# Kernel optimization log

Measured on AMD Instinct MI355X. Metric: run time of the kernel, lower is better.

The kernel has to match this reference:

```python
import jax, jax.numpy as jnp
import numpy as np

B, C, H, W = 1, 96, 128, 128
P = 4            # patch_size
E = 192          # embed_dim
DI = 384         # d_inner = expand * embed_dim
NS = 16          # d_state
R = 12           # dt_rank = ceil(E/16)
K = 4            # scan directions
NBLK = 8         # SS2D_MBs_num
GW = C // 2      # SCPA group width


def layernorm(x, g, b, eps=1e-5):
    mu = x.mean(-1, keepdims=True)
    v = x.var(-1, keepdims=True)
    return (x - mu) * jax.lax.rsqrt(v + eps) * g + b


def batchnorm(x, g, b, m, v, eps=1e-5):
    # eval-mode BatchNorm2d over channel axis 1 of (B,C,H,W)
    return (x - m[:, None, None]) * jax.lax.rsqrt(v + eps)[:, None, None] * g[:, None, None] + b[:, None, None]


def conv2d(x, w):
    return jax.lax.conv_general_dilated(x, w, (1, 1), 'SAME', dimension_numbers=('NCHW', 'OIHW', 'NCHW'))


def dwconv2d(x, w, b):
    out = jax.lax.conv_general_dilated(x, w[:, None], (1, 1), 'SAME',
                                       dimension_numbers=('NCHW', 'OIHW', 'NCHW'),
                                       feature_group_count=w.shape[0])
    return out + b[None, :, None, None]


def lrelu(x):
    return jnp.where(x >= 0, x, 0.2 * x)


def channel_attention(x, w1, w2):
    # CBAM-style: shared MLP on avg+max pooled channel descriptors, sigmoid gate
    avg = x.mean((2, 3))
    mx = x.max((2, 3))
    mlp = lambda v: jax.nn.relu(v @ w1.T) @ w2.T
    attn = jax.nn.sigmoid(mlp(avg) + mlp(mx))
    return x * attn[:, :, None, None]


def selective_scan(xs, dts, A, Bs, Cs, Dskip):
    # xs,dts: (B,K,DI,L); A: (K,DI,NS); Bs,Cs: (B,K,NS,L); Dskip: (K,DI)
    xs_t = jnp.moveaxis(xs, -1, 0)
    dts_t = jnp.moveaxis(dts, -1, 0)
    Bs_t = jnp.moveaxis(Bs, -1, 0)
    Cs_t = jnp.moveaxis(Cs, -1, 0)
    h0 = jnp.zeros(xs.shape[:3] + (NS,), xs.dtype)  # (B,K,DI,NS)

    def step(h, t):
        xt, dt, Bt, Ct = t
        h = jnp.exp(dt[..., None] * A) * h + (dt * xt)[..., None] * Bt[:, :, None, :]
        return h, jnp.sum(h * Ct[:, :, None, :], axis=-1)

    _, ys = jax.lax.scan(step, h0, (xs_t, dts_t, Bs_t, Cs_t))
    return jnp.moveaxis(ys, 0, -1) + xs * Dskip[None, :, :, None]


def ss2d_block(x, p):
    # VMamba-style VSS block: x + SS2D(LN(x)); x: (B,Hp,Wp,E)
    (ln_g, ln_b, inproj_w, conv_w, conv_b, xproj_w, dtproj_w, dtproj_b,
     Alog, Dskip, on_g, on_b, outproj_w, merge_w) = p
    Bsz, Hp, Wp, _ = x.shape
    L = Hp * Wp
    h = layernorm(x, ln_g, ln_b)
    xz = jnp.einsum('bhwd,ed->bhwe', h, inproj_w)   # (B,Hp,Wp,2*DI)
    xc, z = jnp.split(xz, 2, axis=-1)
    xc = jax.nn.silu(dwconv2d(jnp.transpose(xc, (0, 3, 1, 2)), conv_w, conv_b))  # (B,DI,Hp,Wp)
    # 4-direction cross-scan: row-major, col-major and their reverses
    xf = xc.reshape(Bsz, DI, L)
    xwh = jnp.transpose(xc, (0, 1, 3, 2)).reshape(Bsz, DI, L)
    xs = jnp.stack([xf, xwh, jnp.flip(xf, -1), jnp.flip(xwh, -1)], axis=1)  # (B,K,DI,L)
    x_dbl = jnp.einsum('bkdl,kcd->bkcl', xs, xproj_w)  # (B,K,R+2*NS,L)
    dts, Bm, Cm = jnp.split(x_dbl, [R, R + NS], axis=2)
    dts = jax.nn.softplus(jnp.einsum('bkrl,kdr->bkdl', dts, dtproj_w) + dtproj_b[None, :, :, None])
    A = -jnp.exp(Alog)
    oy = selective_scan(xs, dts, A, Bm, Cm, Dskip)  # (B,K,DI,L)
    y0 = oy[:, 0]
    y1 = jnp.transpose(oy[:, 1].reshape(Bsz, DI, Wp, Hp), (0, 1, 3, 2)).reshape(Bsz, DI, L)
    y2 = jnp.flip(oy[:, 2], -1)
    y3 = jnp.transpose(jnp.flip(oy[:, 3], -1).reshape(Bsz, DI, Wp, Hp), (0, 1, 3, 2)).reshape(Bsz, DI, L)
    y = merge_w[0] * y0 + merge_w[1] * y1 + merge_w[2] * y2 + merge_w[3] * y3  # learnable merge
    y = jnp.transpose(y, (0, 2, 1)).reshape(Bsz, Hp, Wp, DI)
    y = layernorm(y, on_g, on_b) * jax.nn.silu(z)
    return x + jnp.einsum('bhwd,ed->bhwe', y, outproj_w)


def scpa(x, c1a, c1b, k1, k2w, k2b, k3, k4, c3):
    # PAN SCPA: two branches (3x3 conv / pixel-attention conv), 1x1 fuse, residual
    a = lrelu(jnp.einsum('bchw,oc->bohw', x, c1a))
    b = lrelu(jnp.einsum('bchw,oc->bohw', x, c1b))
    a = conv2d(a, k1)
    g = jax.nn.sigmoid(jnp.einsum('bchw,oc->bohw', b, k2w) + k2b[None, :, None, None])
    b = conv2d(conv2d(b, k3) * g, k4)
    out = jnp.einsum('bchw,oc->bohw', jnp.concatenate([lrelu(a), lrelu(b)], 1), c3)
    return out + x


def _forward(x, bn1_g, bn1_b, bn1_m, bn1_v, ca_w1, ca_w2, pe_w, pe_b, pu_w, pu_b,
             blk_ln_g, blk_ln_b, blk_inproj_w, blk_conv_w, blk_conv_b, blk_xproj_w,
             blk_dtproj_w, blk_dtproj_b, blk_Alog, blk_D, blk_on_g, blk_on_b,
             blk_outproj_w, blk_merge_w, bn2_g, bn2_b, bn2_m, bn2_v,
             scpa_c1a_w, scpa_c1b_w, scpa_k1_w, pa_k2_w, pa_k2_b, pa_k3_w, pa_k4_w, scpa_c3_w):
    residual = x
    h = batchnorm(x, bn1_g, bn1_b, bn1_m, bn1_v)
    x1 = channel_attention(h, ca_w1, ca_w2)
    Hp, Wp = H // P, W // P
    # patch embed: (B,C,H,W) -> (B,Hp,Wp,C*P*P) -> linear -> (B,Hp,Wp,E)
    xp = h.reshape(B, C, Hp, P, Wp, P).transpose(0, 2, 4, 1, 3, 5).reshape(B, Hp, Wp, C * P * P)
    x2 = xp @ pe_w.T + pe_b
    blk_params = (blk_ln_g, blk_ln_b, blk_inproj_w, blk_conv_w, blk_conv_b, blk_xproj_w,
                  blk_dtproj_w, blk_dtproj_b, blk_Alog, blk_D, blk_on_g, blk_on_b,
                  blk_outproj_w, blk_merge_w)
    x2, _ = jax.lax.scan(lambda c, p: (ss2d_block(c, p), None), x2, blk_params)
    # patch unembed
    xu = x2 @ pu_w.T + pu_b
    xu = xu.reshape(B, Hp, Wp, C, P, P).transpose(0, 3, 1, 4, 2, 5).reshape(B, C, H, W)
    xsum = residual + x1 + xu
    h2 = batchnorm(xsum, bn2_g, bn2_b, bn2_m, bn2_v)
    out = scpa(h2, scpa_c1a_w, scpa_c1b_w, scpa_k1_w, pa_k2_w, pa_k2_b, pa_k3_w, pa_k4_w, scpa_c3_w)
    return out + xsum


def setup_inputs():
    key = jax.random.key(0)
    kct = [0]
    def nk():
        kct[0] += 1
        return jax.random.fold_in(key, kct[0])
    def nrm(shape, s=0.02):
        return (jax.random.normal(nk(), shape) * s).astype(jnp.float32)
    f32 = jnp.float32
    inp = dict(
        x=jax.random.normal(nk(), (B, C, H, W), dtype=f32),
        bn1_g=jnp.ones((C,), f32), bn1_b=jnp.zeros((C,), f32),
        bn1_m=nrm((C,), 0.05), bn1_v=jnp.ones((C,), f32),
        ca_w1=nrm((C // 16, C), 0.1), ca_w2=nrm((C, C // 16), 0.1),
        pe_w=nrm((E, C * P * P)), pe_b=jnp.zeros((E,), f32),
        pu_w=nrm((C * P * P, E)), pu_b=jnp.zeros((C * P * P,), f32),
        blk_ln_g=jnp.ones((NBLK, E), f32), blk_ln_b=jnp.zeros((NBLK, E), f32),
        blk_inproj_w=nrm((NBLK, 2 * DI, E)),
        blk_conv_w=nrm((NBLK, DI, 3, 3), 0.1),
        blk_conv_b=jnp.zeros((NBLK, DI), f32),
        blk_xproj_w=nrm((NBLK, K, R + 2 * NS, DI)),
        blk_dtproj_w=nrm((NBLK, K, DI, R), 0.1),
        blk_dtproj_b=jnp.full((NBLK, K, DI), -4.6, f32),  # softplus ~= 0.01
        blk_Alog=jnp.broadcast_to(jnp.log(jnp.arange(1, NS + 1, dtype=f32)), (NBLK, K, DI, NS)) + 0.0,
        blk_D=jnp.ones((NBLK, K, DI), f32),
        blk_on_g=jnp.ones((NBLK, DI), f32), blk_on_b=jnp.zeros((NBLK, DI), f32),
        blk_outproj_w=nrm((NBLK, E, DI)),
        blk_merge_w=jnp.ones((NBLK, K), f32),
        bn2_g=jnp.ones((C,), f32), bn2_b=jnp.zeros((C,), f32),
        bn2_m=nrm((C,), 0.05), bn2_v=jnp.ones((C,), f32),
        scpa_c1a_w=nrm((GW, C), 0.05), scpa_c1b_w=nrm((GW, C), 0.05),
        scpa_k1_w=nrm((GW, GW, 3, 3), 0.05),
        pa_k2_w=nrm((GW, GW), 0.05), pa_k2_b=jnp.zeros((GW,), f32),
        pa_k3_w=nrm((GW, GW, 3, 3), 0.05), pa_k4_w=nrm((GW, GW, 3, 3), 0.05),
        scpa_c3_w=nrm((C, 2 * GW), 0.05),
    )
    return inp


def reference(x, bn1_g, bn1_b, bn1_m, bn1_v, ca_w1, ca_w2, pe_w, pe_b, pu_w, pu_b,
              blk_ln_g, blk_ln_b, blk_inproj_w, blk_conv_w, blk_conv_b, blk_xproj_w,
              blk_dtproj_w, blk_dtproj_b, blk_Alog, blk_D, blk_on_g, blk_on_b,
              blk_outproj_w, blk_merge_w, bn2_g, bn2_b, bn2_m, bn2_v,
              scpa_c1a_w, scpa_c1b_w, scpa_k1_w, pa_k2_w, pa_k2_b, pa_k3_w, pa_k4_w, scpa_c3_w):
    return _forward(x, bn1_g, bn1_b, bn1_m, bn1_v, ca_w1, ca_w2, pe_w, pe_b, pu_w, pu_b,
                    blk_ln_g, blk_ln_b, blk_inproj_w, blk_conv_w, blk_conv_b, blk_xproj_w,
                    blk_dtproj_w, blk_dtproj_b, blk_Alog, blk_D, blk_on_g, blk_on_b,
                    blk_outproj_w, blk_merge_w, bn2_g, bn2_b, bn2_m, bn2_v,
                    scpa_c1a_w, scpa_c1b_w, scpa_k1_w, pa_k2_w, pa_k2_b, pa_k3_w, pa_k4_w, scpa_c3_w)
```

## Files before the change

kernel.cpp:

```cpp
#include <hip/hip_runtime.h>
#include <math.h>

#define HW 16384
constexpr int C_ = 96;
constexpr int E_ = 192, DI_ = 384, NS_ = 16, R_ = 12, K_ = 4, NBLK_ = 8, GW_ = 48;
constexpr int L_ = 1024, CXP_ = 44;
constexpr int TC_ = 64;
constexpr int NCH_ = L_ / TC_;

__device__ __forceinline__ float lrelu_(float x){ return x >= 0.f ? x : 0.2f*x; }
__device__ __forceinline__ float sigmoid_(float x){ return 1.f/(1.f+expf(-x)); }
__device__ __forceinline__ float silu_(float x){ return x/(1.f+expf(-x)); }
__device__ __forceinline__ float softplus_(float x){ return fmaxf(x,0.f)+log1pf(expf(-fabsf(x))); }

__global__ void k_transpose(const float* __restrict__ in, float* __restrict__ out,
                            int rows, int cols, int in_stride){
  __shared__ float t[32][33];
  const float* ib = in + (size_t)blockIdx.z*rows*in_stride;
  float* ob = out + (size_t)blockIdx.z*rows*cols;
  int r0 = blockIdx.y*32, c0 = blockIdx.x*32;
  int tx = threadIdx.x, ty = threadIdx.y;
  for (int i=0;i<32;i+=8){
    int r = r0+ty+i, c = c0+tx;
    if (r<rows && c<cols) t[ty+i][tx] = ib[(size_t)r*in_stride+c];
  }
  __syncthreads();
  for (int i=0;i<32;i+=8){
    int c = c0+ty+i, r = r0+tx;
    if (r<rows && c<cols) ob[(size_t)c*rows+r] = t[tx][ty+i];
  }
}

__global__ void k_bn1(const float* __restrict__ x, const float* g, const float* b,
                      const float* m, const float* v,
                      float* __restrict__ h, float* __restrict__ stats){
  int c = blockIdx.x, tid = threadIdx.x;
  float sc = g[c]*rsqrtf(v[c]+1e-5f), sh = b[c]-m[c]*sc;
  const float* xc = x + (size_t)c*HW;
  float* hc = h + (size_t)c*HW;
  float s = 0.f, mx = -1e30f;
  for (int i=tid;i<HW;i+=256){
    float val = fmaf(xc[i], sc, sh);
    hc[i] = val; s += val; mx = fmaxf(mx, val);
  }
  for (int o=32;o;o>>=1){ s += __shfl_xor(s,o); mx = fmaxf(mx, __shfl_xor(mx,o)); }
  __shared__ float ss[4], sm[4];
  int wid = tid>>6, lane = tid&63;
  if (!lane){ ss[wid]=s; sm[wid]=mx; }
  __syncthreads();
  if (!tid){
    stats[c] = (ss[0]+ss[1]+ss[2]+ss[3])*(1.f/HW);
    stats[96+c] = fmaxf(fmaxf(sm[0],sm[1]),fmaxf(sm[2],sm[3]));
  }
}

__global__ void k_attn(const float* __restrict__ stats, const float* __restrict__ w1,
                       const float* __restrict__ w2, float* __restrict__ attn){
  __shared__ float hid[12];
  int tid = threadIdx.x;
  if (tid < 12){
    int j = tid%6, which = tid/6;
    const float* vv = stats + which*96;
    float a = 0.f;
    for (int c=0;c<96;c++) a += vv[c]*w1[j*96+c];
    hid[tid] = fmaxf(a, 0.f);
  }
  __syncthreads();
  if (tid < 96){
    float a = 0.f;
    for (int j=0;j<6;j++) a += (hid[j]+hid[6+j])*w2[tid*6+j];
    attn[tid] = sigmoid_(a);
  }
}

__global__ void k_patchify(const float* __restrict__ h, float* __restrict__ xp){
  int idx = blockIdx.x*256 + threadIdx.x;
  int l = idx/1536, kk = idx%1536;
  int c = kk>>4, i = (kk>>2)&3, j = kk&3;
  int hp = l>>5, wp = l&31;
  xp[idx] = h[((size_t)c<<14) + (size_t)(hp*4+i)*128 + (wp*4+j)];
}

__global__ __launch_bounds__(256) void k_gemm32(const float* __restrict__ act,
                      const float* __restrict__ wt, const float* __restrict__ bias,
                      const float* __restrict__ res, float* __restrict__ out,
                      int K, int N){
  __shared__ float As[32][34];
  __shared__ float Bs[32][32];
  int tid = threadIdx.x;
  int m0 = blockIdx.x*32, n0 = blockIdx.y*32;
  int tx = tid&15, ty = tid>>4;
  int arow = tid>>3, akq = tid&7;
  int brow = tid>>3, bn4 = tid&7;
  float4 aR = *(const float4*)&act[(size_t)(m0+arow)*K + akq*4];
  float4 bR = *(const float4*)&wt [(size_t)brow*N + n0 + bn4*4];
  float acc[2][2] = {{0}};
  for (int k0=0; k0<K; k0+=32){
    __syncthreads();
    As[akq*4+0][arow]=aR.x; As[akq*4+1][arow]=aR.y;
    As[akq*4+2][arow]=aR.z; As[akq*4+3][arow]=aR.w;
    *(float4*)&Bs[brow][bn4*4] = bR;
    __syncthreads();
    if (k0+32 < K){
      aR = *(const float4*)&act[(size_t)(m0+arow)*K + k0+32 + akq*4];
      bR = *(const float4*)&wt [(size_t)(k0+32+brow)*N + n0 + bn4*4];
    }
    #pragma unroll
    for (int kk=0; kk<32; kk++){
      float2 av = *(const float2*)&As[kk][ty*2];
      float2 bv = *(const float2*)&Bs[kk][tx*2];
      acc[0][0] = fmaf(av.x, bv.x, acc[0][0]);
      acc[0][1] = fmaf(av.x, bv.y, acc[0][1]);
      acc[1][0] = fmaf(av.y, bv.x, acc[1][0]);
      acc[1][1] = fmaf(av.y, bv.y, acc[1][1]);
    }
  }
  float2 bq = bias ? *(const float2*)&bias[n0+tx*2] : make_float2(0.f,0.f);
  #pragma unroll
  for (int i=0;i<2;i++){
    size_t o = (size_t)(m0+ty*2+i)*N + n0 + tx*2;
    float2 r = res ? *(const float2*)&res[o] : make_float2(0.f,0.f);
    float2 ov;
    ov.x = acc[i][0]+bq.x+r.x; ov.y = acc[i][1]+bq.y+r.y;
    *(float2*)&out[o] = ov;
  }
}

__global__ void k_lnstats(const float* __restrict__ x, float* __restrict__ mu,
                          float* __restrict__ rs){
  int l = blockIdx.x*4 + (threadIdx.x>>6);
  int lane = threadIdx.x&63;
  const float* xr = x + (size_t)l*E_;
  float v0 = xr[lane], v1 = xr[lane+64], v2 = xr[lane+128];
  float s = v0+v1+v2, sq = v0*v0+v1*v1+v2*v2;
  for (int o=32;o;o>>=1){ s += __shfl_xor(s,o); sq += __shfl_xor(sq,o); }
  if (!lane){
    float m = s*(1.f/192.f);
    mu[l] = m;
    rs[l] = rsqrtf(sq*(1.f/192.f) - m*m + 1e-5f);
  }
}

__global__ __launch_bounds__(256) void k_gemm32ln(const float* __restrict__ act,
                      const float* __restrict__ wt, const float* __restrict__ lg,
                      const float* __restrict__ lb, const float* __restrict__ mu,
                      const float* __restrict__ rs, float* __restrict__ out,
                      int K, int N){
  __shared__ float As[32][34];
  __shared__ float Bs[32][32];
  int tid = threadIdx.x;
  int m0 = blockIdx.x*32, n0 = blockIdx.y*32;
  int tx = tid&15, ty = tid>>4;
  int arow = tid>>3, akq = tid&7;
  int brow = tid>>3, bn4 = tid&7;
  float m = mu[m0+arow], r = rs[m0+arow];
  float4 aR = *(const float4*)&act[(size_t)(m0+arow)*K + akq*4];
  float4 gR = *(const float4*)&lg[akq*4];
  float4 hR = *(const float4*)&lb[akq*4];
  float4 bR = *(const float4*)&wt[(size_t)brow*N + n0 + bn4*4];
  float acc[2][2] = {{0}};
  for (int k0=0; k0<K; k0+=32){
    __syncthreads();
    As[akq*4+0][arow] = (aR.x-m)*r*gR.x + hR.x;
    As[akq*4+1][arow] = (aR.y-m)*r*gR.y + hR.y;
    As[akq*4+2][arow] = (aR.z-m)*r*gR.z + hR.z;
    As[akq*4+3][arow] = (aR.w-m)*r*gR.w + hR.w;
    *(float4*)&Bs[brow][bn4*4] = bR;
    __syncthreads();
    if (k0+32 < K){
      aR = *(const float4*)&act[(size_t)(m0+arow)*K + k0+32 + akq*4];
      gR = *(const float4*)&lg[k0+32+akq*4];
      hR = *(const float4*)&lb[k0+32+akq*4];
      bR = *(const float4*)&wt[(size_t)(k0+32+brow)*N + n0 + bn4*4];
    }
    #pragma unroll
    for (int kk=0; kk<32; kk++){
      float2 av = *(const float2*)&As[kk][ty*2];
      float2 bv = *(const float2*)&Bs[kk][tx*2];
      acc[0][0] = fmaf(av.x, bv.x, acc[0][0]);
      acc[0][1] = fmaf(av.x, bv.y, acc[0][1]);
      acc[1][0] = fmaf(av.y, bv.x, acc[1][0]);
      acc[1][1] = fmaf(av.y, bv.y, acc[1][1]);
    }
  }
  #pragma unroll
  for (int i=0;i<2;i++){
    size_t o = (size_t)(m0+ty*2+i)*N + n0 + tx*2;
    float2 ov; ov.x = acc[i][0]; ov.y = acc[i][1];
    *(float2*)&out[o] = ov;
  }
}

__global__ __launch_bounds__(256) void k_dwxst(const float* __restrict__ xz,
                        const float* __restrict__ w, const float* __restrict__ bias,
                        float* __restrict__ xcs, float* __restrict__ xst){
  __shared__ float ld[96][33];
  __shared__ float t[32][33];
  int h0 = blockIdx.x;
  int d0 = blockIdx.y*32;
  int tx = threadIdx.x, ty = threadIdx.y;
  #pragma unroll
  for (int i=0;i<12;i++){
    int ll = i*8 + ty;
    int h = h0 - 1 + (ll>>5);
    int wv = ll & 31;
    float v = 0.f;
    if ((unsigned)h < 32u) v = xz[(size_t)(h*32+wv)*768 + d0 + tx];
    ld[ll][tx] = v;
  }
  __syncthreads();
  #pragma unroll
  for (int i=0;i<4;i++){
    int dl = ty + 8*i;
    int d = d0 + dl;
    float acc = bias[d];
    const float* wp = w + d*9;
    #pragma unroll
    for (int di=0;di<3;di++){
      #pragma unroll
      for (int dj=0;dj<3;dj++){
        int wq = tx + dj - 1;
        if ((unsigned)wq < 32u)
          acc = fmaf(ld[di*32 + wq][dl], wp[di*3+dj], acc);
      }
    }
    float val = silu_(acc);
    xcs[(size_t)d*L_ + h0*32 + tx] = val;
    t[dl][tx] = val;
  }
  __syncthreads();
  int d = d0 + tx;
  #pragma unroll
  for (int i=0;i<4;i++){
    int wq = ty + 8*i;
    int l = h0*32 + wq;
    float val = t[tx][wq];
    int t1 = wq*32 + h0;
    xst[(size_t)l*DI_ + d] = val;
    xst[(size_t)(L_ + t1)*DI_ + d] = val;
    xst[(size_t)(2*L_ + (1023-l))*DI_ + d] = val;
    xst[(size_t)(3*L_ + (1023-t1))*DI_ + d] = val;
  }
}

__global__ __launch_bounds__(256) void k_xdblP(const float* __restrict__ xcs,
                       const float* __restrict__ xw, float* __restrict__ xdblP){
  int kz = blockIdx.z;
  int k = kz & 3, sp = kz >> 2;
  int s = blockIdx.x*256 + threadIdx.x;
  int Ts = ((s&31)<<5) | (s>>5);
  int lw;
  if (k==0) lw = s;
  else if (k==1) lw = Ts;
  else if (k==2) lw = 1023-s;
  else lw = 1023-Ts;
  int c0 = blockIdx.y*4;
  const float* wp = xw + ((size_t)k*CXP_ + c0)*DI_ + sp*128;
  const float* src = xcs + s + (size_t)sp*128*L_;
  float a0=0,a1=0,a2=0,a3=0;
  for (int d=0; d<128; d++){
    float v = src[(size_t)d*L_];
    a0 = fmaf(v, wp[d],        a0);
    a1 = fmaf(v, wp[DI_+d],    a1);
    a2 = fmaf(v, wp[2*DI_+d],  a2);
    a3 = fmaf(v, wp[3*DI_+d],  a3);
  }
  size_t base = (((size_t)sp*4 + k)*CXP_ + c0)*L_ + lw;
  xdblP[base]       = a0;
  xdblP[base+L_]    = a1;
  xdblP[base+2*L_]  = a2;
  xdblP[base+3*L_]  = a3;
}

__global__ void k_dtbc(const float* __restrict__ xdblP, const float* __restrict__ dtw,
                       const float* __restrict__ dtb, float* __restrict__ dts_t,
                       float* __restrict__ bc){
  int k = blockIdx.y, l = blockIdx.x, d = threadIdx.x;
  const float* p0 = xdblP + ((size_t)(0+k)*CXP_)*L_ + l;
  const float* p1 = xdblP + ((size_t)(4+k)*CXP_)*L_ + l;
  const float* p2 = xdblP + ((size_t)(8+k)*CXP_)*L_ + l;
  float acc = dtb[(size_t)k*DI_ + d];
  const float* w = dtw + ((size_t)k*DI_ + d)*R_;
  #pragma unroll
  for (int r=0;r<R_;r++){
    size_t o = (size_t)r*L_;
    acc = fmaf(p0[o]+p1[o]+p2[o], w[r], acc);
  }
  dts_t[((size_t)k*L_ + l)*DI_ + d] = softplus_(acc);
  if (d < 32){
    size_t o = (size_t)(R_+d)*L_;
    bc[((size_t)k*L_ + l)*32 + d] = p0[o]+p1[o]+p2[o];
  }
}

__global__ __launch_bounds__(256) void k_scanA(const float* __restrict__ xst,
                      const float* __restrict__ dts_t, const float* __restrict__ bc,
                      const float* __restrict__ Alog,
                      float* __restrict__ Ech, float* __restrict__ Hch){
  int k = blockIdx.z;
  int d = blockIdx.y*16 + (threadIdx.x>>4);
  int n = threadIdx.x&15;
  int ch = blockIdx.x;
  float A = -expf(Alog[((size_t)k*DI_ + d)*NS_ + n]);
  float aL2 = A * 1.4426950408889634f;
  int t0 = ch*TC_;
  const float* dtp = dts_t + ((size_t)k*L_ + t0)*DI_ + d;
  const float* xp_ = xst   + ((size_t)k*L_ + t0)*DI_ + d;
  const float* bcp = bc    + ((size_t)k*L_ + t0)*32;
  float h = 0.f, Ep = 1.f;
  #pragma unroll 4
  for (int t=0;t<TC_;t++){
    float dt = dtp[(size_t)t*DI_];
    float xv = xp_[(size_t)t*DI_];
    float Bn = bcp[t*32+n];
    float e = exp2f(aL2*dt);
    h = fmaf(e, h, dt*xv*Bn);
    Ep *= e;
  }
  size_t idx = (((size_t)k*NCH_ + ch)*DI_ + d)*NS_ + n;
  Ech[idx] = Ep; Hch[idx] = h;
}

__global__ void k_scanB(const float* __restrict__ Ech, const float* __restrict__ Hch,
                        float* __restrict__ carry){
  int idx = blockIdx.x*256 + threadIdx.x;
  int k = idx / (DI_*NS_);
  int dn = idx % (DI_*NS_);
  float h = 0.f;
  #pragma unroll
  for (int c=0;c<NCH_;c++){
    size_t o = ((size_t)(k*NCH_+c)*DI_*NS_) + dn;
    carry[o] = h;
    h = fmaf(Ech[o], h, Hch[o]);
  }
}

__global__ __launch_bounds__(256) void k_scanC(const float* __restrict__ xst,
                      const float* __restrict__ dts_t, const float* __restrict__ bc,
                      const float* __restrict__ Alog, const float* __restrict__ carry,
                      float* __restrict__ yst){
  int k = blockIdx.z;
  int d = blockIdx.y*16 + (threadIdx.x>>4);
  int n = threadIdx.x&15;
  int ch = blockIdx.x;
  float A = -expf(Alog[((size_t)k*DI_ + d)*NS_ + n]);
  float aL2 = A * 1.4426950408889634f;
  int t0 = ch*TC_;
  const float* dtp = dts_t + ((size_t)k*L_ + t0)*DI_ + d;
  const float* xp_ = xst   + ((size_t)k*L_ + t0)*DI_ + d;
  const float* bcp = bc    + ((size_t)k*L_ + t0)*32;
  float* yp = yst + ((size_t)k*L_ + t0)*DI_ + d;
  float h = carry[(((size_t)k*NCH_ + ch)*DI_ + d)*NS_ + n];
  #pragma unroll 4
  for (int t=0;t<TC_;t++){
    float dt = dtp[(size_t)t*DI_];
    float xv = xp_[(size_t)t*DI_];
    float Bn = bcp[t*32+n], Cn = bcp[t*32+16+n];
    float e = exp2f(aL2*dt);
    h = fmaf(e, h, dt*xv*Bn);
    float p = h*Cn;
    p += __shfl_xor(p,1); p += __shfl_xor(p,2);
    p += __shfl_xor(p,4); p += __shfl_xor(p,8);
    if (n==0) yp[(size_t)t*DI_] = p;
  }
}

__global__ void k_merge(const float* __restrict__ yst, const float* __restrict__ xst,
                        const float* __restrict__ Dsk, const float* __restrict__ mw,
                        const float* __restrict__ ong, const float* __restrict__ onb,
                        const float* __restrict__ xz, float* __restrict__ out){
  int l = blockIdx.x, d = threadIdx.x;
  int T = ((l&31)<<5) | (l>>5);
  int tt[4] = { l, T, 1023-l, 1023-T };
  float v = 0.f;
  #pragma unroll
  for (int k=0;k<4;k++){
    size_t idx = (size_t)(k*L_ + tt[k])*DI_ + d;
    v += mw[k]*(yst[idx] + xst[idx]*Dsk[k*DI_+d]);
  }
  float s = v, sq = v*v;
  for (int o=32;o;o>>=1){ s += __shfl_xor(s,o); sq += __shfl_xor(sq,o); }
  __shared__ float rs_[6], rq_[6];
  int lane = d&63, wid = d>>6;
  if (!lane){ rs_[wid]=s; rq_[wid]=sq; }
  __syncthreads();
  float ts=0.f, tq=0.f;
  #pragma unroll
  for (int i=0;i<6;i++){ ts += rs_[i]; tq += rq_[i]; }
  float mu = ts*(1.f/DI_);
  float rstd = rsqrtf(tq*(1.f/DI_) - mu*mu + 1e-5f);
  float y = (v-mu)*rstd*ong[d] + onb[d];
  float z = xz[(size_t)l*768 + DI_ + d];
  out[(size_t)l*DI_ + d] = y * silu_(z);
}

__global__ void k_sum(const float* __restrict__ x, const float* __restrict__ h,
                      const float* __restrict__ attn, const float* __restrict__ xu,
                      const float* g2, const float* b2, const float* m2, const float* v2,
                      float* __restrict__ xsum, float* __restrict__ h2){
  int idx = blockIdx.x*256 + threadIdx.x;
  int c = idx>>14, p = idx&16383;
  int hh = p>>7, ww = p&127;
  int l = (hh>>2)*32 + (ww>>2);
  int o = (c<<4) + ((hh&3)<<2) + (ww&3);
  float s = x[idx] + h[idx]*attn[c] + xu[(size_t)l*1536 + o];
  xsum[idx] = s;
  h2[idx] = (s - m2[c])*rsqrtf(v2[c]+1e-5f)*g2[c] + b2[c];
}

__global__ __launch_bounds__(256) void k_1x1ab(const float* __restrict__ h2,
                        const float* __restrict__ wa, const float* __restrict__ wb,
                        float* __restrict__ a, float* __restrict__ b){
  __shared__ float lw[96*12];
  int ocg = blockIdx.x;
  for (int i=threadIdx.x; i<96*12; i+=256){
    int o = i%12, c = i/12;
    lw[i] = (o<6) ? wa[(ocg*6 + o)*96 + c] : wb[(ocg*6 + (o-6))*96 + c];
  }
  __syncthreads();
  int p = blockIdx.y*256 + threadIdx.x;
  float acc[12];
  #pragma unroll
  for (int o=0;o<12;o++) acc[o]=0.f;
  for (int c=0;c<96;c++){
    float v = h2[(size_t)c*HW + p];
    const float* w = lw + c*12;
    #pragma unroll
    for (int o=0;o<12;o++) acc[o] = fmaf(v, w[o], acc[o]);
  }
  #pragma unroll
  for (int o=0;o<6;o++){
    a[(size_t)(ocg*6+o)*HW + p] = lrelu_(acc[o]);
    b[(size_t)(ocg*6+o)*HW + p] = lrelu_(acc[6+o]);
  }
}

__global__ __launch_bounds__(256) void k_1x1g(const float* __restrict__ b,
                       const float* __restrict__ w, const float* __restrict__ bias,
                       float* __restrict__ g){
  __shared__ float lw[48*6];
  int ocg = blockIdx.x;
  for (int i=threadIdx.x; i<48*6; i+=256){
    int o = i%6, c = i/6;
    lw[i] = w[(ocg*6 + o)*48 + c];
  }
  __syncthreads();
  int p = blockIdx.y*256 + threadIdx.x;
  float acc[6];
  #pragma unroll
  for (int o=0;o<6;o++) acc[o] = bias[ocg*6+o];
  for (int c=0;c<48;c++){
    float v = b[(size_t)c*HW + p];
    const float* wp = lw + c*6;
    #pragma unroll
    for (int o=0;o<6;o++) acc[o] = fmaf(v, wp[o], acc[o]);
  }
  #pragma unroll
  for (int o=0;o<6;o++) g[(size_t)(ocg*6+o)*HW + p] = sigmoid_(acc[o]);
}

__global__ __launch_bounds__(256) void k_conv3(const float* __restrict__ in,
                        const float* __restrict__ w, const float* __restrict__ aux,
                        float* __restrict__ out, int mode){
  __shared__ float lw[48*9*6];
  int ocg = blockIdx.x;
  for (int i=threadIdx.x; i<48*9*6; i+=256){
    int o = i%6, j = (i/6)%9, ic = i/54;
    lw[i] = w[((size_t)(ocg*6+o)*48 + ic)*9 + j];
  }
  __syncthreads();
  int p = blockIdx.y*256 + threadIdx.x;
  int hh = p>>7, ww = p&127;
  float acc[6];
  #pragma unroll
  for (int o=0;o<6;o++) acc[o]=0.f;
  for (int ic=0; ic<48; ic++){
    const float* ip = in + (size_t)ic*HW;
    float xv[9];
    #pragma unroll
    for (int di=0;di<3;di++){
      int y = hh+di-1;
      bool yok = (unsigned)y < 128u;
      #pragma unroll
      for (int dj=0;dj<3;dj++){
        int xx = ww+dj-1;
        bool ok = yok && ((unsigned)xx < 128u);
        xv[di*3+dj] = ok ? ip[y*128+xx] : 0.f;
      }
    }
    const float* lwp = lw + ic*54;
    #pragma unroll
    for (int j=0;j<9;j++){
      float xj = xv[j];
      const float* wj = lwp + j*6;
      #pragma unroll
      for (int o=0;o<6;o++) acc[o] = fmaf(xj, wj[o], acc[o]);
    }
  }
  #pragma unroll
  for (int o=0;o<6;o++){
    size_t oi = (size_t)(ocg*6+o)*HW + p;
    out[oi] = (mode==0) ? lrelu_(acc[o]) : acc[o]*aux[oi];
  }
}

__global__ __launch_bounds__(256) void k_c3(const float* __restrict__ ab,
                     const float* __restrict__ w, const float* __restrict__ h2,
                     const float* __restrict__ xsum, float* __restrict__ out){
  __shared__ float lw[96*12];
  int ocg = blockIdx.x;
  for (int i=threadIdx.x; i<96*12; i+=256){
    int o = i%12, j = i/12;
    lw[i] = w[(ocg*12 + o)*96 + j];
  }
  __syncthreads();
  int p = blockIdx.y*256 + threadIdx.x;
  float acc[12];
  #pragma unroll
  for (int o=0;o<12;o++) acc[o]=0.f;
  for (int j=0;j<96;j++){
    float v = ab[(size_t)j*HW + p];
    const float* wp = lw + j*12;
    #pragma unroll
    for (int o=0;o<12;o++) acc[o] = fmaf(v, wp[o], acc[o]);
  }
  #pragma unroll
  for (int o=0;o<12;o++){
    size_t oi = (size_t)(ocg*12+o)*HW + p;
    out[oi] = acc[o] + h2[oi] + xsum[oi];
  }
}

extern "C" void kernel_launch(void* const* d_in, const int* in_sizes, int n_in,
                              void* d_out, int out_size, void* d_ws, size_t ws_size,
                              hipStream_t stream){
  (void)in_sizes; (void)n_in; (void)out_size; (void)ws_size;
  const float* x    = (const float*)d_in[0];
  const float* bn1g = (const float*)d_in[1];
  const float* bn1b = (const float*)d_in[2];
  const float* bn1m = (const float*)d_in[3];
  const float* bn1v = (const float*)d_in[4];
  const float* caw1 = (const float*)d_in[5];
  const float* caw2 = (const float*)d_in[6];
  const float* peW  = (const float*)d_in[7];
  const float* peb  = (const float*)d_in[8];
  const float* puW  = (const float*)d_in[9];
  const float* pub  = (const float*)d_in[10];
  const float* lng  = (const float*)d_in[11];
  const float* lnb  = (const float*)d_in[12];
  const float* inW  = (const float*)d_in[13];
  const float* convw= (const float*)d_in[14];
  const float* convb= (const float*)d_in[15];
  const float* xprojw=(const float*)d_in[16];
  const float* dtw  = (const float*)d_in[17];
  const float* dtb  = (const float*)d_in[18];
  const float* Alog = (const float*)d_in[19];
  const float* Dsk  = (const float*)d_in[20];
  const float* ong  = (const float*)d_in[21];
  const float* onb  = (const float*)d_in[22];
  const float* outW = (const float*)d_in[23];
  const float* mw   = (const float*)d_in[24];
  const float* bn2g = (const float*)d_in[25];
  const float* bn2b = (const float*)d_in[26];
  const float* bn2m = (const float*)d_in[27];
  const float* bn2v = (const float*)d_in[28];
  const float* c1a  = (const float*)d_in[29];
  const float* c1b  = (const float*)d_in[30];
  const float* k1w  = (const float*)d_in[31];
  const float* k2w  = (const float*)d_in[32];
  const float* k2b  = (const float*)d_in[33];
  const float* k3w  = (const float*)d_in[34];
  const float* k4w  = (const float*)d_in[35];
  const float* c3w  = (const float*)d_in[36];
  float* out = (float*)d_out;

  float* ws = (float*)d_ws;
  size_t off = 0;
  auto alloc = [&](size_t n){ float* p = ws + off; off += n; return p; };
  float* peWT  = alloc((size_t)1536*192);
  float* puWT  = alloc((size_t)192*1536);
  float* inWT  = alloc((size_t)8*192*768);
  float* outWT = alloc((size_t)8*384*192);
  float* bufH  = alloc((size_t)96*HW);
  float* stats = alloc(256);
  float* attn  = alloc(128);
  float* bufP  = alloc((size_t)1024*1536);
  float* x2a   = alloc((size_t)1024*192);
  float* x2b   = alloc((size_t)1024*192);
  float* bufXZ = alloc((size_t)1024*768);
  float* bufXCS= alloc((size_t)384*1024);
  float* bufXST= alloc((size_t)4*1024*384);
  float* xdblP = alloc((size_t)12*44*1024);
  float* dts   = alloc((size_t)4*1024*384);
  float* bc    = alloc((size_t)4*1024*32);
  float* yst   = alloc((size_t)4*1024*384);
  float* bufY  = alloc((size_t)1024*384);
  float* xsum  = alloc((size_t)96*HW);
  float* h2    = alloc((size_t)96*HW);
  float* Ech   = alloc((size_t)K_*NCH_*DI_*NS_);
  float* Hch   = alloc((size_t)K_*NCH_*DI_*NS_);
  float* carry = alloc((size_t)K_*NCH_*DI_*NS_);
  float* muB   = alloc(1024);
  float* rsB   = alloc(1024);

  dim3 tb(32,8);
  k_transpose<<<dim3(48,6,1), tb, 0, stream>>>(peW, peWT, 192, 1536, 1536);
  k_transpose<<<dim3(6,48,1), tb, 0, stream>>>(puW, puWT, 1536, 192, 192);
  k_transpose<<<dim3(6,24,8), tb, 0, stream>>>(inW, inWT, 768, 192, 192);
  k_transpose<<<dim3(12,6,8), tb, 0, stream>>>(outW, outWT, 192, 384, 384);

  k_bn1<<<96,256,0,stream>>>(x, bn1g, bn1b, bn1m, bn1v, bufH, stats);
  k_attn<<<1,128,0,stream>>>(stats, caw1, caw2, attn);
  k_patchify<<<(1024*1536)/256,256,0,stream>>>(bufH, bufP);
  k_gemm32<<<dim3(32,6),256,0,stream>>>(bufP, peWT, peb, nullptr, x2a, 1536, 192);

  float* cur = x2a; float* nxt = x2b;
  for (int b=0;b<8;b++){
    k_lnstats<<<256,256,0,stream>>>(cur, muB, rsB);
    k_gemm32ln<<<dim3(32,24),256,0,stream>>>(cur, inWT+(size_t)b*192*768,
                        lng+(size_t)b*192, lnb+(size_t)b*192, muB, rsB, bufXZ, 192, 768);
    k_dwxst<<<dim3(32,12),tb,0,stream>>>(bufXZ, convw+(size_t)b*384*9,
                        convb+(size_t)b*384, bufXCS, bufXST);
    k_xdblP<<<dim3(4,11,12),256,0,stream>>>(bufXCS, xprojw+(size_t)b*4*44*384, xdblP);
    k_dtbc<<<dim3(1024,4),384,0,stream>>>(xdblP, dtw+(size_t)b*4*384*12, dtb+(size_t)b*4*384, dts, bc);
    const float* Ab = Alog + (size_t)b*4*384*16;
    k_scanA<<<dim3(NCH_,DI_/16,4),256,0,stream>>>(bufXST, dts, bc, Ab, Ech, Hch);
    k_scanB<<<(K_*DI_*NS_)/256,256,0,stream>>>(Ech, Hch, carry);
    k_scanC<<<dim3(NCH_,DI_/16,4),256,0,stream>>>(bufXST, dts, bc, Ab, carry, yst);
    k_merge<<<1024,384,0,stream>>>(yst, bufXST, Dsk+(size_t)b*4*384, mw+(size_t)b*4,
                                   ong+(size_t)b*384, onb+(size_t)b*384, bufXZ, bufY);
    k_gemm32<<<dim3(32,6),256,0,stream>>>(bufY, outWT+(size_t)b*384*192, nullptr, cur, nxt, 384, 192);
    float* t = cur; cur = nxt; nxt = t;
  }

  k_gemm32<<<dim3(32,48),256,0,stream>>>(cur, puWT, pub, nullptr, bufP, 192, 1536);
  k_sum<<<(96*HW)/256,256,0,stream>>>(x, bufH, attn, bufP, bn2g, bn2b, bn2m, bn2v, xsum, h2);

  float* bufA = dts;
  float* bufB = dts + (size_t)48*HW;
  float* bufG = yst;
  float* bufT = yst + (size_t)48*HW;
  float* ab   = bufXST;
  k_1x1ab<<<dim3(8,64),256,0,stream>>>(h2, c1a, c1b, bufA, bufB);
  k_1x1g<<<dim3(8,64),256,0,stream>>>(bufB, k2w, k2b, bufG);
  k_conv3<<<dim3(8,64),256,0,stream>>>(bufA, k1w, nullptr, ab, 0);
  k_conv3<<<dim3(8,64),256,0,stream>>>(bufB, k3w, bufG, bufT, 1);
  k_conv3<<<dim3(8,64),256,0,stream>>>(bufT, k4w, nullptr, ab+(size_t)48*HW, 0);
  k_c3<<<dim3(8,64),256,0,stream>>>(ab, c3w, h2, xsum, out);
}
```

Before: 1.161 ms.

## Fuse patchify, unpatchify and LN stats into GEMMs; dedupe scan inputs; tile conv3 in LDS

Several independent changes land together. Patchify is folded into the patch-embed GEMM's A loads, and the unpatchify scatter is moved into the patch-unembed GEMM's epilogue. The per-block LayerNorm statistics kernel is removed: row sum and sum-of-squares are accumulated with atomics in the residual GEMM epilogue, and the merge kernel zeroes the accumulators for the next use. The four direction-permuted copies of the scan input become two, with reversed directions read via a negative stride. The 3x3 conv now stages input rows in shared memory. Together these cut launches and memory traffic, at the cost of atomics, an E[x^2]-m^2 variance form, and extra per-channel syncs in the conv.

```diff
diff --git a/kernel.cpp b/kernel.cpp
--- a/kernel.cpp
+++ b/kernel.cpp
@@ -33,8 +33,11 @@
 
 __global__ void k_bn1(const float* __restrict__ x, const float* g, const float* b,
                       const float* m, const float* v,
-                      float* __restrict__ h, float* __restrict__ stats){
+                      float* __restrict__ h, float* __restrict__ stats,
+                      float* __restrict__ su, float* __restrict__ sq){
   int c = blockIdx.x, tid = threadIdx.x;
+  int gid = c*256 + tid;
+  if (gid < 1024){ su[gid] = 0.f; sq[gid] = 0.f; }
   float sc = g[c]*rsqrtf(v[c]+1e-5f), sh = b[c]-m[c]*sc;
   const float* xc = x + (size_t)c*HW;
   float* hc = h + (size_t)c*HW;
@@ -73,17 +76,69 @@
   }
 }
 
-__global__ void k_patchify(const float* __restrict__ h, float* __restrict__ xp){
-  int idx = blockIdx.x*256 + threadIdx.x;
-  int l = idx/1536, kk = idx%1536;
-  int c = kk>>4, i = (kk>>2)&3, j = kk&3;
-  int hp = l>>5, wp = l&31;
-  xp[idx] = h[((size_t)c<<14) + (size_t)(hp*4+i)*128 + (wp*4+j)];
-}
-
-__global__ __launch_bounds__(256) void k_gemm32(const float* __restrict__ act,
+__global__ __launch_bounds__(256) void k_gemmPE(const float* __restrict__ hsrc,
                       const float* __restrict__ wt, const float* __restrict__ bias,
-                      const float* __restrict__ res, float* __restrict__ out,
+                      float* __restrict__ out, float* __restrict__ su, float* __restrict__ sq){
+  const int K = 1536, N = 192;
+  __shared__ float As[32][34];
+  __shared__ float Bs[32][32];
+  int tid = threadIdx.x;
+  int m0 = blockIdx.x*32, n0 = blockIdx.y*32;
+  int tx = tid&15, ty = tid>>4;
+  int arow = tid>>3, akq = tid&7;
+  int brow = tid>>3, bn4 = tid&7;
+  int m = m0+arow;
+  int base2 = (m>>5)*512 + (m&31)*4;
+  auto aload = [&](int kk)->float4 {
+    int c = kk>>4, i2 = (kk>>2)&3;
+    return *(const float4*)&hsrc[((size_t)c<<14) + (size_t)(i2*128 + base2)];
+  };
+  float4 aR = aload(akq*4);
+  float4 bR = *(const float4*)&wt[(size_t)brow*N + n0 + bn4*4];
+  float acc[2][2] = {{0}};
+  for (int k0=0; k0<K; k0+=32){
+    __syncthreads();
+    As[akq*4+0][arow]=aR.x; As[akq*4+1][arow]=aR.y;
+    As[akq*4+2][arow]=aR.z; As[akq*4+3][arow]=aR.w;
+    *(float4*)&Bs[brow][bn4*4] = bR;
+    __syncthreads();
+    if (k0+32 < K){
+      aR = aload(k0+32+akq*4);
+      bR = *(const float4*)&wt[(size_t)(k0+32+brow)*N + n0 + bn4*4];
+    }
+    #pragma unroll
+    for (int kk=0; kk<32; kk++){
+      float2 av = *(const float2*)&As[kk][ty*2];
+      float2 bv = *(const float2*)&Bs[kk][tx*2];
+      acc[0][0] = fmaf(av.x, bv.x, acc[0][0]);
+      acc[0][1] = fmaf(av.x, bv.y, acc[0][1]);
+      acc[1][0] = fmaf(av.y, bv.x, acc[1][0]);
+      acc[1][1] = fmaf(av.y, bv.y, acc[1][1]);
+    }
+  }
+  float2 bq = *(const float2*)&bias[n0+tx*2];
+  float sl[2], ql[2];
+  #pragma unroll
+  for (int i=0;i<2;i++){
+    size_t o = (size_t)(m0+ty*2+i)*N + n0 + tx*2;
+    float2 ov; ov.x = acc[i][0]+bq.x; ov.y = acc[i][1]+bq.y;
+    *(float2*)&out[o] = ov;
+    sl[i] = ov.x+ov.y; ql[i] = ov.x*ov.x+ov.y*ov.y;
+  }
+  #pragma unroll
+  for (int o=8;o;o>>=1){
+    sl[0]+=__shfl_xor(sl[0],o); ql[0]+=__shfl_xor(ql[0],o);
+    sl[1]+=__shfl_xor(sl[1],o); ql[1]+=__shfl_xor(ql[1],o);
+  }
+  if (tx==0){
+    atomicAdd(&su[m0+ty*2],   sl[0]); atomicAdd(&sq[m0+ty*2],   ql[0]);
+    atomicAdd(&su[m0+ty*2+1], sl[1]); atomicAdd(&sq[m0+ty*2+1], ql[1]);
+  }
+}
+
+__global__ __launch_bounds__(256) void k_gemm32s(const float* __restrict__ act,
+                      const float* __restrict__ wt, const float* __restrict__ res,
+                      float* __restrict__ out, float* __restrict__ su, float* __restrict__ sq,
                       int K, int N){
   __shared__ float As[32][34];
   __shared__ float Bs[32][32];
@@ -115,36 +170,76 @@
       acc[1][1] = fmaf(av.y, bv.y, acc[1][1]);
     }
   }
-  float2 bq = bias ? *(const float2*)&bias[n0+tx*2] : make_float2(0.f,0.f);
+  float sl[2], ql[2];
   #pragma unroll
   for (int i=0;i<2;i++){
     size_t o = (size_t)(m0+ty*2+i)*N + n0 + tx*2;
-    float2 r = res ? *(const float2*)&res[o] : make_float2(0.f,0.f);
-    float2 ov;
-    ov.x = acc[i][0]+bq.x+r.x; ov.y = acc[i][1]+bq.y+r.y;
+    float2 r = *(const float2*)&res[o];
+    float2 ov; ov.x = acc[i][0]+r.x; ov.y = acc[i][1]+r.y;
     *(float2*)&out[o] = ov;
-  }
-}
-
-__global__ void k_lnstats(const float* __restrict__ x, float* __restrict__ mu,
-                          float* __restrict__ rs){
-  int l = blockIdx.x*4 + (threadIdx.x>>6);
-  int lane = threadIdx.x&63;
-  const float* xr = x + (size_t)l*E_;
-  float v0 = xr[lane], v1 = xr[lane+64], v2 = xr[lane+128];
-  float s = v0+v1+v2, sq = v0*v0+v1*v1+v2*v2;
-  for (int o=32;o;o>>=1){ s += __shfl_xor(s,o); sq += __shfl_xor(sq,o); }
-  if (!lane){
-    float m = s*(1.f/192.f);
-    mu[l] = m;
-    rs[l] = rsqrtf(sq*(1.f/192.f) - m*m + 1e-5f);
+    sl[i] = ov.x+ov.y; ql[i] = ov.x*ov.x+ov.y*ov.y;
+  }
+  #pragma unroll
+  for (int o=8;o;o>>=1){
+    sl[0]+=__shfl_xor(sl[0],o); ql[0]+=__shfl_xor(ql[0],o);
+    sl[1]+=__shfl_xor(sl[1],o); ql[1]+=__shfl_xor(ql[1],o);
+  }
+  if (tx==0){
+    atomicAdd(&su[m0+ty*2],   sl[0]); atomicAdd(&sq[m0+ty*2],   ql[0]);
+    atomicAdd(&su[m0+ty*2+1], sl[1]); atomicAdd(&sq[m0+ty*2+1], ql[1]);
+  }
+}
+
+__global__ __launch_bounds__(256) void k_gemmPU(const float* __restrict__ act,
+                      const float* __restrict__ wt, const float* __restrict__ bias,
+                      float* __restrict__ out){
+  const int K = 192, N = 1536;
+  __shared__ float As[32][34];
+  __shared__ float Bs[32][32];
+  int tid = threadIdx.x;
+  int m0 = blockIdx.x*32, n0 = blockIdx.y*32;
+  int tx = tid&15, ty = tid>>4;
+  int arow = tid>>3, akq = tid&7;
+  int brow = tid>>3, bn4 = tid&7;
+  float4 aR = *(const float4*)&act[(size_t)(m0+arow)*K + akq*4];
+  float4 bR = *(const float4*)&wt [(size_t)brow*N + n0 + bn4*4];
+  float acc[2][2] = {{0}};
+  for (int k0=0; k0<K; k0+=32){
+    __syncthreads();
+    As[akq*4+0][arow]=aR.x; As[akq*4+1][arow]=aR.y;
+    As[akq*4+2][arow]=aR.z; As[akq*4+3][arow]=aR.w;
+    *(float4*)&Bs[brow][bn4*4] = bR;
+    __syncthreads();
+    if (k0+32 < K){
+      aR = *(const float4*)&act[(size_t)(m0+arow)*K + k0+32 + akq*4];
+      bR = *(const float4*)&wt [(size_t)(k0+32+brow)*N + n0 + bn4*4];
+    }
+    #pragma unroll
+    for (int kk=0; kk<32; kk++){
+      float2 av = *(const float2*)&As[kk][ty*2];
+      float2 bv = *(const float2*)&Bs[kk][tx*2];
+      acc[0][0] = fmaf(av.x, bv.x, acc[0][0]);
+      acc[0][1] = fmaf(av.x, bv.y, acc[0][1]);
+      acc[1][0] = fmaf(av.y, bv.x, acc[1][0]);
+      acc[1][1] = fmaf(av.y, bv.y, acc[1][1]);
+    }
+  }
+  int n = n0 + tx*2;
+  float2 bq = *(const float2*)&bias[n];
+  int c = n>>4, i2 = (n>>2)&3, j = n&3;
+  #pragma unroll
+  for (int i=0;i<2;i++){
+    int m = m0+ty*2+i;
+    size_t o = ((size_t)c<<14) + (size_t)((m>>5)*4+i2)*128 + (m&31)*4 + j;
+    float2 ov; ov.x = acc[i][0]+bq.x; ov.y = acc[i][1]+bq.y;
+    *(float2*)&out[o] = ov;
   }
 }
 
 __global__ __launch_bounds__(256) void k_gemm32ln(const float* __restrict__ act,
                       const float* __restrict__ wt, const float* __restrict__ lg,
-                      const float* __restrict__ lb, const float* __restrict__ mu,
-                      const float* __restrict__ rs, float* __restrict__ out,
+                      const float* __restrict__ lb, const float* __restrict__ su,
+                      const float* __restrict__ sq, float* __restrict__ out,
                       int K, int N){
   __shared__ float As[32][34];
   __shared__ float Bs[32][32];
@@ -153,7 +248,8 @@
   int tx = tid&15, ty = tid>>4;
   int arow = tid>>3, akq = tid&7;
   int brow = tid>>3, bn4 = tid&7;
-  float m = mu[m0+arow], r = rs[m0+arow];
+  float m = su[m0+arow]*(1.f/192.f);
+  float r = rsqrtf(sq[m0+arow]*(1.f/192.f) - m*m + 1e-5f);
   float4 aR = *(const float4*)&act[(size_t)(m0+arow)*K + akq*4];
   float4 gR = *(const float4*)&lg[akq*4];
   float4 hR = *(const float4*)&lb[akq*4];
@@ -193,7 +289,8 @@
 
 __global__ __launch_bounds__(256) void k_dwxst(const float* __restrict__ xz,
                         const float* __restrict__ w, const float* __restrict__ bias,
-                        float* __restrict__ xcs, float* __restrict__ xst){
+                        float* __restrict__ xcs, float* __restrict__ xst0,
+                        float* __restrict__ xst1){
   __shared__ float ld[96][33];
   __shared__ float t[32][33];
   int h0 = blockIdx.x;
@@ -236,10 +333,8 @@
     int l = h0*32 + wq;
     float val = t[tx][wq];
     int t1 = wq*32 + h0;
-    xst[(size_t)l*DI_ + d] = val;
-    xst[(size_t)(L_ + t1)*DI_ + d] = val;
-    xst[(size_t)(2*L_ + (1023-l))*DI_ + d] = val;
-    xst[(size_t)(3*L_ + (1023-t1))*DI_ + d] = val;
+    xst0[(size_t)l*DI_ + d] = val;
+    xst1[(size_t)t1*DI_ + d] = val;
   }
 }
 
@@ -293,7 +388,8 @@
   }
 }
 
-__global__ __launch_bounds__(256) void k_scanA(const float* __restrict__ xst,
+__global__ __launch_bounds__(256) void k_scanA(const float* __restrict__ xst0,
+                      const float* __restrict__ xst1,
                       const float* __restrict__ dts_t, const float* __restrict__ bc,
                       const float* __restrict__ Alog,
                       float* __restrict__ Ech, float* __restrict__ Hch){
@@ -305,13 +401,16 @@
   float aL2 = A * 1.4426950408889634f;
   int t0 = ch*TC_;
   const float* dtp = dts_t + ((size_t)k*L_ + t0)*DI_ + d;
-  const float* xp_ = xst   + ((size_t)k*L_ + t0)*DI_ + d;
   const float* bcp = bc    + ((size_t)k*L_ + t0)*32;
+  const float* xb = (k&1) ? xst1 : xst0;
+  const float* xp_; ptrdiff_t xs_;
+  if (k < 2){ xp_ = xb + (size_t)t0*DI_ + d; xs_ = DI_; }
+  else      { xp_ = xb + (size_t)(1023-t0)*DI_ + d; xs_ = -(ptrdiff_t)DI_; }
   float h = 0.f, Ep = 1.f;
   #pragma unroll 4
   for (int t=0;t<TC_;t++){
     float dt = dtp[(size_t)t*DI_];
-    float xv = xp_[(size_t)t*DI_];
+    float xv = xp_[(ptrdiff_t)t*xs_];
     float Bn = bcp[t*32+n];
     float e = exp2f(aL2*dt);
     h = fmaf(e, h, dt*xv*Bn);
@@ -335,7 +434,8 @@
   }
 }
 
-__global__ __launch_bounds__(256) void k_scanC(const float* __restrict__ xst,
+__global__ __launch_bounds__(256) void k_scanC(const float* __restrict__ xst0,
+                      const float* __restrict__ xst1,
                       const float* __restrict__ dts_t, const float* __restrict__ bc,
                       const float* __restrict__ Alog, const float* __restrict__ carry,
                       float* __restrict__ yst){
@@ -347,14 +447,17 @@
   float aL2 = A * 1.4426950408889634f;
   int t0 = ch*TC_;
   const float* dtp = dts_t + ((size_t)k*L_ + t0)*DI_ + d;
-  const float* xp_ = xst   + ((size_t)k*L_ + t0)*DI_ + d;
   const float* bcp = bc    + ((size_t)k*L_ + t0)*32;
+  const float* xb = (k&1) ? xst1 : xst0;
+  const float* xp_; ptrdiff_t xs_;
+  if (k < 2){ xp_ = xb + (size_t)t0*DI_ + d; xs_ = DI_; }
+  else      { xp_ = xb + (size_t)(1023-t0)*DI_ + d; xs_ = -(ptrdiff_t)DI_; }
   float* yp = yst + ((size_t)k*L_ + t0)*DI_ + d;
   float h = carry[(((size_t)k*NCH_ + ch)*DI_ + d)*NS_ + n];
   #pragma unroll 4
   for (int t=0;t<TC_;t++){
     float dt = dtp[(size_t)t*DI_];
-    float xv = xp_[(size_t)t*DI_];
+    float xv = xp_[(ptrdiff_t)t*xs_];
     float Bn = bcp[t*32+n], Cn = bcp[t*32+16+n];
     float e = exp2f(aL2*dt);
     h = fmaf(e, h, dt*xv*Bn);
@@ -365,24 +468,29 @@
   }
 }
 
-__global__ void k_merge(const float* __restrict__ yst, const float* __restrict__ xst,
+__global__ void k_merge(const float* __restrict__ yst, const float* __restrict__ xst0,
+                        const float* __restrict__ xst1,
                         const float* __restrict__ Dsk, const float* __restrict__ mw,
                         const float* __restrict__ ong, const float* __restrict__ onb,
-                        const float* __restrict__ xz, float* __restrict__ out){
+                        const float* __restrict__ xz, float* __restrict__ out,
+                        float* __restrict__ su, float* __restrict__ sq){
   int l = blockIdx.x, d = threadIdx.x;
+  if (d == 0){ su[l] = 0.f; sq[l] = 0.f; }
   int T = ((l&31)<<5) | (l>>5);
   int tt[4] = { l, T, 1023-l, 1023-T };
+  float xv0 = xst0[(size_t)l*DI_ + d];
+  float xv1 = xst1[(size_t)T*DI_ + d];
   float v = 0.f;
   #pragma unroll
   for (int k=0;k<4;k++){
-    size_t idx = (size_t)(k*L_ + tt[k])*DI_ + d;
-    v += mw[k]*(yst[idx] + xst[idx]*Dsk[k*DI_+d]);
-  }
-  float s = v, sq = v*v;
-  for (int o=32;o;o>>=1){ s += __shfl_xor(s,o); sq += __shfl_xor(sq,o); }
+    float xk = (k&1) ? xv1 : xv0;
+    v += mw[k]*(yst[(size_t)(k*L_ + tt[k])*DI_ + d] + xk*Dsk[k*DI_+d]);
+  }
+  float s = v, sqv = v*v;
+  for (int o=32;o;o>>=1){ s += __shfl_xor(s,o); sqv += __shfl_xor(sqv,o); }
   __shared__ float rs_[6], rq_[6];
   int lane = d&63, wid = d>>6;
-  if (!lane){ rs_[wid]=s; rq_[wid]=sq; }
+  if (!lane){ rs_[wid]=s; rq_[wid]=sqv; }
   __syncthreads();
   float ts=0.f, tq=0.f;
   #pragma unroll
@@ -399,11 +507,8 @@
                       const float* g2, const float* b2, const float* m2, const float* v2,
                       float* __restrict__ xsum, float* __restrict__ h2){
   int idx = blockIdx.x*256 + threadIdx.x;
-  int c = idx>>14, p = idx&16383;
-  int hh = p>>7, ww = p&127;
-  int l = (hh>>2)*32 + (ww>>2);
-  int o = (c<<4) + ((hh&3)<<2) + (ww&3);
-  float s = x[idx] + h[idx]*attn[c] + xu[(size_t)l*1536 + o];
+  int c = idx>>14;
+  float s = x[idx] + h[idx]*attn[c] + xu[idx];
   xsum[idx] = s;
   h2[idx] = (s - m2[c])*rsqrtf(v2[c]+1e-5f)*g2[c] + b2[c];
 }
@@ -463,38 +568,40 @@
                         const float* __restrict__ w, const float* __restrict__ aux,
                         float* __restrict__ out, int mode){
   __shared__ float lw[48*9*6];
+  __shared__ float ld[4][128];
   int ocg = blockIdx.x;
   for (int i=threadIdx.x; i<48*9*6; i+=256){
     int o = i%6, j = (i/6)%9, ic = i/54;
     lw[i] = w[((size_t)(ocg*6+o)*48 + ic)*9 + j];
   }
-  __syncthreads();
   int p = blockIdx.y*256 + threadIdx.x;
-  int hh = p>>7, ww = p&127;
+  int ww = p&127;
+  int hbase = blockIdx.y*2 - 1;
+  int lr = 1 + (threadIdx.x>>7);
   float acc[6];
   #pragma unroll
   for (int o=0;o<6;o++) acc[o]=0.f;
   for (int ic=0; ic<48; ic++){
-    const float* ip = in + (size_t)ic*HW;
-    float xv[9];
+    __syncthreads();
+    #pragma unroll
+    for (int q=0;q<2;q++){
+      int idx = threadIdx.x + q*256;
+      int r = idx>>7, cp = idx&127;
+      int gy = hbase + r;
+      ld[r][cp] = ((unsigned)gy < 128u) ? in[(size_t)ic*HW + gy*128 + cp] : 0.f;
+    }
+    __syncthreads();
+    const float* lwp = lw + ic*54;
     #pragma unroll
     for (int di=0;di<3;di++){
-      int y = hh+di-1;
-      bool yok = (unsigned)y < 128u;
       #pragma unroll
       for (int dj=0;dj<3;dj++){
         int xx = ww+dj-1;
-        bool ok = yok && ((unsigned)xx < 128u);
-        xv[di*3+dj] = ok ? ip[y*128+xx] : 0.f;
+        float xv = ((unsigned)xx < 128u) ? ld[lr-1+di][xx] : 0.f;
+        const float* wj = lwp + (di*3+dj)*6;
+        #pragma unroll
+        for (int o=0;o<6;o++) acc[o] = fmaf(xv, wj[o], acc[o]);
       }
-    }
-    const float* lwp = lw + ic*54;
-    #pragma unroll
-    for (int j=0;j<9;j++){
-      float xj = xv[j];
-      const float* wj = lwp + j*6;
-      #pragma unroll
-      for (int o=0;o<6;o++) acc[o] = fmaf(xj, wj[o], acc[o]);
     }
   }
   #pragma unroll
@@ -600,8 +707,10 @@
   float* Ech   = alloc((size_t)K_*NCH_*DI_*NS_);
   float* Hch   = alloc((size_t)K_*NCH_*DI_*NS_);
   float* carry = alloc((size_t)K_*NCH_*DI_*NS_);
-  float* muB   = alloc(1024);
-  float* rsB   = alloc(1024);
+  float* suB   = alloc(1024);
+  float* sqB   = alloc(1024);
+  float* xst0  = bufXST;
+  float* xst1  = bufXST + (size_t)L_*DI_;
 
   dim3 tb(32,8);
   k_transpose<<<dim3(48,6,1), tb, 0, stream>>>(peW, peWT, 192, 1536, 1536);
@@ -609,31 +718,29 @@
   k_transpose<<<dim3(6,24,8), tb, 0, stream>>>(inW, inWT, 768, 192, 192);
   k_transpose<<<dim3(12,6,8), tb, 0, stream>>>(outW, outWT, 192, 384, 384);
 
-  k_bn1<<<96,256,0,stream>>>(x, bn1g, bn1b, bn1m, bn1v, bufH, stats);
+  k_bn1<<<96,256,0,stream>>>(x, bn1g, bn1b, bn1m, bn1v, bufH, stats, suB, sqB);
   k_attn<<<1,128,0,stream>>>(stats, caw1, caw2, attn);
-  k_patchify<<<(1024*1536)/256,256,0,stream>>>(bufH, bufP);
-  k_gemm32<<<dim3(32,6),256,0,stream>>>(bufP, peWT, peb, nullptr, x2a, 1536, 192);
+  k_gemmPE<<<dim3(32,6),256,0,stream>>>(bufH, peWT, peb, x2a, suB, sqB);
 
   float* cur = x2a; float* nxt = x2b;
   for (int b=0;b<8;b++){
-    k_lnstats<<<256,256,0,stream>>>(cur, muB, rsB);
     k_gemm32ln<<<dim3(32,24),256,0,stream>>>(cur, inWT+(size_t)b*192*768,
-                        lng+(size_t)b*192, lnb+(size_t)b*192, muB, rsB, bufXZ, 192, 768);
+                        lng+(size_t)b*192, lnb+(size_t)b*192, suB, sqB, bufXZ, 192, 768);
     k_dwxst<<<dim3(32,12),tb,0,stream>>>(bufXZ, convw+(size_t)b*384*9,
-                        convb+(size_t)b*384, bufXCS, bufXST);
+                        convb+(size_t)b*384, bufXCS, xst0, xst1);
     k_xdblP<<<dim3(4,11,12),256,0,stream>>>(bufXCS, xprojw+(size_t)b*4*44*384, xdblP);
     k_dtbc<<<dim3(1024,4),384,0,stream>>>(xdblP, dtw+(size_t)b*4*384*12, dtb+(size_t)b*4*384, dts, bc);
     const float* Ab = Alog + (size_t)b*4*384*16;
-    k_scanA<<<dim3(NCH_,DI_/16,4),256,0,stream>>>(bufXST, dts, bc, Ab, Ech, Hch);
+    k_scanA<<<dim3(NCH_,DI_/16,4),256,0,stream>>>(xst0, xst1, dts, bc, Ab, Ech, Hch);
     k_scanB<<<(K_*DI_*NS_)/256,256,0,stream>>>(Ech, Hch, carry);
-    k_scanC<<<dim3(NCH_,DI_/16,4),256,0,stream>>>(bufXST, dts, bc, Ab, carry, yst);
-    k_merge<<<1024,384,0,stream>>>(yst, bufXST, Dsk+(size_t)b*4*384, mw+(size_t)b*4,
-                                   ong+(size_t)b*384, onb+(size_t)b*384, bufXZ, bufY);
-    k_gemm32<<<dim3(32,6),256,0,stream>>>(bufY, outWT+(size_t)b*384*192, nullptr, cur, nxt, 384, 192);
+    k_scanC<<<dim3(NCH_,DI_/16,4),256,0,stream>>>(xst0, xst1, dts, bc, Ab, carry, yst);
+    k_merge<<<1024,384,0,stream>>>(yst, xst0, xst1, Dsk+(size_t)b*4*384, mw+(size_t)b*4,
+                                   ong+(size_t)b*384, onb+(size_t)b*384, bufXZ, bufY, suB, sqB);
+    k_gemm32s<<<dim3(32,6),256,0,stream>>>(bufY, outWT+(size_t)b*384*192, cur, nxt, suB, sqB, 384, 192);
     float* t = cur; cur = nxt; nxt = t;
   }
 
-  k_gemm32<<<dim3(32,48),256,0,stream>>>(cur, puWT, pub, nullptr, bufP, 192, 1536);
+  k_gemmPU<<<dim3(32,48),256,0,stream>>>(cur, puWT, pub, bufP);
   k_sum<<<(96*HW)/256,256,0,stream>>>(x, bufH, attn, bufP, bn2g, bn2b, bn2m, bn2v, xsum, h2);
 
   float* bufA = dts;
```

Measured after the change: 1.203 ms. +3.7%, slower.
